# Kernel tuning notes

Hardware: AMD Instinct MI355X
Metric: run time of the kernel (lower is better)

Reference implementation:

```python
import jax, jax.numpy as jnp
import numpy as np

# --- FineRMoE routing constants (match init_kwargs) ---
TOP_K = 4
G_I, G_O = 2, 2
R_I, R_O = 4, 2
NUM_EXPERTS = 32  # must equal R_O*G_O*R_I*G_I


def _finermoe_router(scores):
    """scores: [T, E]. Returns (probs [T,top_k], selected [T,top_k])."""
    T, E = scores.shape
    S = E // (R_O * G_O)  # experts per concat-shard == R_I*G_I
    cs = scores.reshape(T, R_O * G_O, S)
    # top_k//G_O experts within each (R_O*G_O) shard
    _, add_idx = jax.lax.top_k(cs, TOP_K // G_O)
    add_mask = jnp.any(jax.nn.one_hot(add_idx, S, dtype=bool), axis=-2)  # [T, RO*GO, S]
    # keep the max-scoring R_O shard within each G_O group (argmax -> first max, like torch)
    shard_sum = cs.sum(-1).reshape(T, G_O, R_O)
    concat_mask = jax.nn.one_hot(jnp.argmax(shard_sum, axis=-1), R_O, dtype=bool)
    concat_mask = concat_mask.reshape(T, G_O * R_O)  # flat order matches RO*GO shard dim
    final_mask = (add_mask & concat_mask[:, :, None]).reshape(T, E)
    masked = jnp.where(final_mask, scores, -jnp.inf)
    probs, sel = jax.lax.top_k(masked, TOP_K)
    return probs, sel


def setup_inputs() -> dict:
    key = jax.random.key(0)
    ks = jax.random.split(key, 6)
    B, Sq, H, E, I = 1, 2048, 1024, NUM_EXPERTS, 256
    O = H // G_O  # expert output width
    return {
        "hidden_states": jax.random.normal(ks[0], (B, Sq, H), dtype=jnp.float32),
        "Wr": jax.random.normal(ks[1], (H, E), dtype=jnp.float32) * 0.02,
        "Wg": jax.random.normal(ks[2], (E, H, I), dtype=jnp.float32) * 0.02,
        "Wu": jax.random.normal(ks[3], (E, H, I), dtype=jnp.float32) * 0.02,
        "Wd": jax.random.normal(ks[4], (E, I, O), dtype=jnp.float32) * 0.02,
        "Wc": jax.random.normal(ks[5], (H, H), dtype=jnp.float32) * 0.02,
    }


def reference(hidden_states, Wr, Wg, Wu, Wd, Wc):
    B, Sq, H = hidden_states.shape
    T = B * Sq
    E = Wr.shape[1]
    x = hidden_states.reshape(T, H)
    router_logits = x @ Wr  # [T, E]
    probs, sel = _finermoe_router(router_logits)
    rw = jax.nn.softmax(probs.astype(jnp.float32), axis=1)
    rw = rw / rw.sum(-1, keepdims=True)  # norm_topk_prob
    rw = rw.astype(x.dtype)
    # dense combine weights [T, E] (zero for unselected experts)
    C = jnp.zeros((T, E), x.dtype).at[jnp.arange(T)[:, None], sel].add(rw)
    # all-expert MLP (stacked GEMMs); combine weights mask out unselected tokens
    h = jax.nn.silu(jnp.einsum('th,ehi->eti', x, Wg)) * jnp.einsum('th,ehi->eti', x, Wu)
    y = jnp.einsum('eti,eio->eto', h, Wd)  # [E, T, H//G_O]
    P = E // G_O  # experts per concat shard slice == R_O*G_I*R_I
    out = jnp.einsum('tgp,gpto->tgo', C.reshape(T, G_O, P),
                     y.reshape(G_O, P, T, H // G_O)).reshape(T, H)
    out = out @ Wc  # moe_concat_proj
    return out.reshape(B, Sq, H), router_logits
```

## Files before the change

### kernel.cpp

```cpp
#include <hip/hip_runtime.h>
#include <hip/hip_bf16.h>
#include <math.h>
#include <stdint.h>

typedef __hip_bfloat16 hbf16;

#define T_TOK 2048
#define H_DIM 1024
#define E_NUM 32
#define I_DIM 256
#define O_DIM 512
#define CAP   2048
#define TT    16
#define WT    16
#define XSTR2 520
#define HSTR  264
#define CSTR  32

typedef __bf16 bf16x8 __attribute__((ext_vector_type(8)));
typedef float  f32x4  __attribute__((ext_vector_type(4)));

__device__ __forceinline__ float b2f(hbf16 v) { return __bfloat162float(v); }
__device__ __forceinline__ float bb2f(ushort u) { return __uint_as_float((uint32_t)u << 16); }

__device__ __forceinline__ ushort f2b(float f) {
    uint32_t u = __float_as_uint(f);
    return (ushort)((u + 0x7FFFu + ((u >> 16) & 1u)) >> 16);
}

template<int BF>
__device__ __forceinline__ float ld(const void* p, size_t i) {
    if (BF) return b2f(((const hbf16*)p)[i]);
    else    return ((const float*)p)[i];
}

__device__ __forceinline__ f32x4 mfma_bf16(bf16x8 a, bf16x8 b, f32x4 c) {
    return __builtin_amdgcn_mfma_f32_16x16x32_bf16(a, b, c, 0, 0, 0);
}

__device__ __forceinline__ void sched_fence() { __builtin_amdgcn_sched_barrier(0); }

__global__ __launch_bounds__(256) void detect_kernel(
    const uint32_t* __restrict__ xw, int* __restrict__ flag, int* __restrict__ counts)
{
    __shared__ int cnt;
    if (threadIdx.x == 0) cnt = 0;
    if (threadIdx.x < E_NUM) counts[threadIdx.x * CSTR] = 0;
    __syncthreads();
    int c = 0;
    for (int i = threadIdx.x; i < 1024; i += 256) {
        int e = (xw[i] >> 7) & 0xFF;
        if (e >= 110 && e <= 140) c++;
    }
    atomicAdd(&cnt, c);
    __syncthreads();
    if (threadIdx.x == 0) *flag = (cnt > 512) ? 1 : 0;
}


__device__ void conv3_tile(const void* __restrict__ src, ushort* __restrict__ dst,
                           int bf, int K, int N, int b, float* __restrict__ sh)
{
    int tilesN = N >> 7, tilesK = K >> 5;
    int e  = b / (tilesK * tilesN);
    int r  = b % (tilesK * tilesN);
    int k0 = (r / tilesN) << 5;
    int n0 = (r % tilesN) << 7;
    size_t base = (size_t)e * K * N;
    int tid = threadIdx.x;
    {
        int row = tid >> 3, c0 = (tid & 7) * 16;
        if (!bf) {
            const float* sp = (const float*)src + base + (size_t)(k0 + row) * N + n0 + c0;
            #pragma unroll
            for (int i = 0; i < 4; ++i) {
                float4 v = *(const float4*)(sp + i * 4);
                sh[row * 132 + c0 + i*4 + 0] = v.x;
                sh[row * 132 + c0 + i*4 + 1] = v.y;
                sh[row * 132 + c0 + i*4 + 2] = v.z;
                sh[row * 132 + c0 + i*4 + 3] = v.w;
            }
        } else {
            const hbf16* sp = (const hbf16*)src + base + (size_t)(k0 + row) * N + n0 + c0;
            #pragma unroll
            for (int i = 0; i < 16; ++i) sh[row * 132 + c0 + i] = b2f(sp[i]);
        }
    }
    __syncthreads();
    {
        int nn = tid >> 1, kk = (tid & 1) * 16;
        union { ushort v[16]; uint4 u[2]; } R;
        #pragma unroll
        for (int i = 0; i < 16; ++i) R.v[i] = f2b(sh[(kk + i) * 132 + nn]);
        ushort* dp = dst + base + ((size_t)(k0 >> 5) * N + (n0 + nn)) * 32 + kk;
        *(uint4*)dp       = R.u[0];
        *(uint4*)(dp + 8) = R.u[1];
    }
    __syncthreads();
}

template<int BF>
__device__ void router3_body(const void* __restrict__ x, const void* __restrict__ Wr,
                             void* __restrict__ out_base,
                             int* __restrict__ counts, int* __restrict__ tok_list,
                             float* __restrict__ wt_list,
                             float* __restrict__ xs, float* __restrict__ sl,
                             float* __restrict__ sf, int t0)
{
    int tid  = threadIdx.x;
    int e    = tid & 31;
    int half = tid >> 5;

    {
        int t = tid >> 7;
        int c = (tid & 127) * 8;
        if (!BF) {
            const float* xp = (const float*)x + (size_t)(t0 + t) * H_DIM + c;
            *(float4*)&xs[t*1024 + c]     = *(const float4*)xp;
            *(float4*)&xs[t*1024 + c + 4] = *(const float4*)(xp + 4);
        } else {
            const hbf16* xp = (const hbf16*)x + (size_t)(t0 + t) * H_DIM + c;
            #pragma unroll
            for (int j = 0; j < 8; ++j) xs[t*1024 + c + j] = b2f(xp[j]);
        }
    }
    __syncthreads();

    float a0 = 0.f, a1 = 0.f;
    int kbase = half * 128;
    const float* xr0 = &xs[kbase];
    const float* xr1 = &xs[1024 + kbase];
    #pragma unroll 8
    for (int k = 0; k < 128; ++k) {
        float w = ld<BF>(Wr, (size_t)(kbase + k) * E_NUM + e);
        a0 = fmaf(xr0[k], w, a0);
        a1 = fmaf(xr1[k], w, a1);
    }
    sl[(0*8 + half)*32 + e] = a0;
    sl[(1*8 + half)*32 + e] = a1;
    __syncthreads();

    if (tid < 64) {
        int t  = tid >> 5;
        int ee = tid & 31;
        float s = 0.f;
        #pragma unroll
        for (int h = 0; h < 8; ++h) s += sl[(t*8 + h)*32 + ee];
        sf[t*32 + ee] = s;
        size_t li = (size_t)T_TOK * H_DIM + (size_t)(t0 + t) * E_NUM + ee;
        if (BF) ((hbf16*)out_base)[li] = __float2bfloat16(s);
        else    ((float*)out_base)[li] = s;
    }
    __syncthreads();

    if (tid < 2) {
        int t = t0 + tid;
        float s[E_NUM];
        #pragma unroll
        for (int i = 0; i < E_NUM; ++i) s[i] = sf[tid * 32 + i];

        int   selE[4];
        float selL[4];
        int ns = 0;
        for (int g = 0; g < 2; ++g) {
            float sum0 = 0.f, sum1 = 0.f;
            #pragma unroll
            for (int j = 0; j < 8; ++j) {
                sum0 += s[(2*g)   * 8 + j];
                sum1 += s[(2*g+1) * 8 + j];
            }
            int bestSh = (sum1 > sum0) ? (2*g+1) : (2*g);
            int base = bestSh * 8;
            int i1 = 0;
            for (int j = 1; j < 8; ++j) if (s[base+j] > s[base+i1]) i1 = j;
            int i2 = -1;
            for (int j = 0; j < 8; ++j) {
                if (j == i1) continue;
                if (i2 < 0 || s[base+j] > s[base+i2]) i2 = j;
            }
            selE[ns] = base + i1; selL[ns] = s[base+i1]; ++ns;
            selE[ns] = base + i2; selL[ns] = s[base+i2]; ++ns;
        }
        float m = fmaxf(fmaxf(selL[0], selL[1]), fmaxf(selL[2], selL[3]));
        float w[4];
        float sum = 0.f;
        for (int j = 0; j < 4; ++j) { w[j] = expf(selL[j] - m); sum += w[j]; }
        float inv = 1.f / sum;
        for (int j = 0; j < 4; ++j) {
            int ee = selE[j];
            int pos = atomicAdd(&counts[ee * CSTR], 1);
            if (pos >= 0 && pos < CAP) {
                tok_list[ee * CAP + pos] = t | (j << 11);
                wt_list[ee * CAP + pos]  = w[j] * inv;
            }
        }
    }
}

__global__ __launch_bounds__(256) void fused_cr_kernel(
    const void* x, const void* Wr,
    const void* Wg, const void* Wu, const void* Wd, const void* Wc,
    ushort* Wg_t, ushort* Wu_t, ushort* Wd_t, ushort* Wc_t,
    void* out_base, const int* __restrict__ flag,
    int* counts, int* tok_list, float* wt_list)
{
    __shared__ __align__(16) float sh[32 * 132];
    int b = blockIdx.x;
    if (b < 1024) {
        float* xs = sh;
        float* sl = sh + 2048;
        float* sf = sh + 2560;
        if (*flag) router3_body<1>(x, Wr, out_base, counts, tok_list, wt_list,
                                   xs, sl, sf, b * 2);
        else       router3_body<0>(x, Wr, out_base, counts, tok_list, wt_list,
                                   xs, sl, sf, b * 2);
    } else {
        int bb = b - 1024;
        int bf = *flag;
        if      (bb < 2048) conv3_tile(Wg, Wg_t, bf, 1024,  256, bb,        sh);
        else if (bb < 4096) conv3_tile(Wu, Wu_t, bf, 1024,  256, bb - 2048, sh);
        else if (bb < 5120) conv3_tile(Wd, Wd_t, bf,  256,  512, bb - 4096, sh);
        else                conv3_tile(Wc, Wc_t, bf, 1024, 1024, bb - 5120, sh);
    }
}

template<int BF>
__device__ void expert3_body(const void* __restrict__ x,
    const ushort* __restrict__ Wg_t, const ushort* __restrict__ Wu_t,
    const ushort* __restrict__ Wd_t,
    const int* __restrict__ counts, const int* __restrict__ tok_list,
    const float* __restrict__ wt_list, ushort* __restrict__ ybuf,
    ushort* __restrict__ xA, ushort* __restrict__ hsm,
    int* __restrict__ tokid, float* __restrict__ twt, int* __restrict__ tslot)
{
    int e = blockIdx.x;
    int n = counts[e * CSTR]; n = n < 0 ? 0 : (n > CAP ? CAP : n);
    int t0 = blockIdx.y * 32;
    if (t0 >= n) return;
    int tid  = threadIdx.x;
    int lane = tid & 63, wv = tid >> 6;
    int q = lane >> 4, l15 = lane & 15;

    if (tid < 32) {
        int it = t0 + tid;
        int id; float ww;
        if (it < n) { id = tok_list[e*CAP + it]; ww = wt_list[e*CAP + it]; }
        else        { id = tok_list[e*CAP + t0]; ww = 0.f; }
        tokid[tid] = id & 2047;
        tslot[tid] = (id >> 11) & 3;
        twt[tid]   = ww;
    }
    __syncthreads();

    const ushort* Bg0 = Wg_t + (size_t)e * (H_DIM * I_DIM) + (wv*32 + l15) * 32 + q*8;
    const ushort* Bu0 = Wu_t + (size_t)e * (H_DIM * I_DIM) + (wv*32 + l15) * 32 + q*8;

    f32x4 Cg[2][2], Cu[2][2];
    #pragma unroll
    for (int m = 0; m < 2; ++m)
        #pragma unroll
        for (int j = 0; j < 2; ++j) { Cg[m][j] = (f32x4)0.f; Cu[m][j] = (f32x4)0.f; }

    bf16x8 bg[2][4][2], bu[2][4][2];
    #pragma unroll
    for (int ig = 0; ig < 4; ++ig)
        #pragma unroll
        for (int j = 0; j < 2; ++j) {
            bg[0][ig][j] = *(const bf16x8*)(Bg0 + (size_t)ig*8192 + j*512);
            bu[0][ig][j] = *(const bf16x8*)(Bu0 + (size_t)ig*8192 + j*512);
        }
    sched_fence();

    #pragma unroll
    for (int hk = 0; hk < 2; ++hk) {
        if (hk) __syncthreads();

        {
            int row = tid >> 4;
            int kb  = (tid & 15) * 8;
            size_t srow = (size_t)tokid[row] * H_DIM + hk * 512;
            #pragma unroll
            for (int c = 0; c < 4; ++c) {
                int k = kb + c * 128;
                union { ushort v[8]; uint4 u; } U;
                if (BF) {
                    U.u = *(const uint4*)((const ushort*)x + srow + k);
                } else {
                    const float* xp = (const float*)x + srow + k;
                    float4 a = *(const float4*)xp;
                    float4 b = *(const float4*)(xp + 4);
                    U.v[0]=f2b(a.x); U.v[1]=f2b(a.y); U.v[2]=f2b(a.z); U.v[3]=f2b(a.w);
                    U.v[4]=f2b(b.x); U.v[5]=f2b(b.y); U.v[6]=f2b(b.z); U.v[7]=f2b(b.w);
                }
                *(uint4*)&xA[row * XSTR2 + k] = U.u;
            }
        }
        __syncthreads();

        #pragma unroll
        for (int g2 = 0; g2 < 4; ++g2) {
            int grp = hk * 4 + g2;
            int cb  = grp & 1;
            if (grp < 7) {
                #pragma unroll
                for (int ig = 0; ig < 4; ++ig)
                    #pragma unroll
                    for (int j = 0; j < 2; ++j) {
                        int idx = (grp + 1) * 4 + ig;
                        bg[cb^1][ig][j] = *(const bf16x8*)(Bg0 + (size_t)idx*8192 + j*512);
                        bu[cb^1][ig][j] = *(const bf16x8*)(Bu0 + (size_t)idx*8192 + j*512);
                    }
            }
            sched_fence();
            #pragma unroll
            for (int ig = 0; ig < 4; ++ig) {
                int kl = (g2 * 4 + ig) * 32;
                bf16x8 A0 = *(const bf16x8*)&xA[(l15)      * XSTR2 + kl + q*8];
                bf16x8 A1 = *(const bf16x8*)&xA[(16 + l15) * XSTR2 + kl + q*8];
                #pragma unroll
                for (int j = 0; j < 2; ++j) {
                    Cg[0][j] = mfma_bf16(A0, bg[cb][ig][j], Cg[0][j]);
                    Cg[1][j] = mfma_bf16(A1, bg[cb][ig][j], Cg[1][j]);
                    Cu[0][j] = mfma_bf16(A0, bu[cb][ig][j], Cu[0][j]);
                    Cu[1][j] = mfma_bf16(A1, bu[cb][ig][j], Cu[1][j]);
                }
            }
        }
    }

    const ushort* Bd0 = Wd_t + (size_t)e * (I_DIM * O_DIM) + (wv*64 + l15) * 32 + q*8;
    bf16x8 bd[2][4][4];
    #pragma unroll
    for (int g2 = 0; g2 < 2; ++g2)
        #pragma unroll
        for (int kc2 = 0; kc2 < 4; ++kc2)
            #pragma unroll
            for (int j = 0; j < 4; ++j)
                bd[g2][kc2][j] = *(const bf16x8*)(Bd0 + (size_t)(g2*4 + kc2)*16384 + j*512);
    sched_fence();

    #pragma unroll
    for (int m = 0; m < 2; ++m)
        #pragma unroll
        for (int j = 0; j < 2; ++j)
            #pragma unroll
            for (int r = 0; r < 4; ++r) {
                float g = Cg[m][j][r], u = Cu[m][j][r];
                float h = (g / (1.f + expf(-g))) * u;
                hsm[(m*16 + q*4 + r) * HSTR + wv*32 + j*16 + l15] = f2b(h);
            }
    __syncthreads();

    f32x4 Cd[2][4];
    #pragma unroll
    for (int m = 0; m < 2; ++m)
        #pragma unroll
        for (int j = 0; j < 4; ++j) Cd[m][j] = (f32x4)0.f;

    #pragma unroll
    for (int g2 = 0; g2 < 2; ++g2)
        #pragma unroll
        for (int kc2 = 0; kc2 < 4; ++kc2) {
            int kc = g2 * 4 + kc2;
            bf16x8 A0 = *(const bf16x8*)&hsm[(l15)      * HSTR + kc*32 + q*8];
            bf16x8 A1 = *(const bf16x8*)&hsm[(16 + l15) * HSTR + kc*32 + q*8];
            #pragma unroll
            for (int j = 0; j < 4; ++j) {
                Cd[0][j] = mfma_bf16(A0, bd[g2][kc2][j], Cd[0][j]);
                Cd[1][j] = mfma_bf16(A1, bd[g2][kc2][j], Cd[1][j]);
            }
        }

    #pragma unroll
    for (int m = 0; m < 2; ++m)
        #pragma unroll
        for (int r = 0; r < 4; ++r) {
            int row = m*16 + q*4 + r;
            if (t0 + row < n) {
                float ww = twt[row];
                size_t base = ((size_t)tokid[row] * 4 + tslot[row]) * O_DIM;
                #pragma unroll
                for (int j = 0; j < 4; ++j)
                    ybuf[base + wv*64 + j*16 + l15] = f2b(ww * Cd[m][j][r]);
            }
        }
}

__global__ __launch_bounds__(512, 2) void expert3_kernel(
    const void* x, const ushort* Wg_t, const ushort* Wu_t, const ushort* Wd_t,
    const int* flag, const int* counts, const int* tok_list, const float* wt_list,
    ushort* ybuf)
{
    __shared__ ushort xA[32 * XSTR2];
    __shared__ ushort hsm[32 * HSTR];
    __shared__ int    tokid[32];
    __shared__ float  twt[32];
    __shared__ int    tslot[32];
    if (*flag) expert3_body<1>(x, Wg_t, Wu_t, Wd_t, counts, tok_list, wt_list,
                               ybuf, xA, hsm, tokid, twt, tslot);
    else       expert3_body<0>(x, Wg_t, Wu_t, Wd_t, counts, tok_list, wt_list,
                               ybuf, xA, hsm, tokid, twt, tslot);
}

template<int BF>
__device__ void wc3_body(const ushort* __restrict__ ybuf, const ushort* __restrict__ Wc_t,
                         void* __restrict__ out_base, ushort* __restrict__ zA)
{
    int m0  = blockIdx.x * 32;
    int n0  = blockIdx.y * 256;
    int tid = threadIdx.x;
    int lane = tid & 63, wv = tid >> 6;
    int q = lane >> 4, l15 = lane & 15;

    const ushort* Bc0 = Wc_t + (size_t)(n0 + wv*32 + l15) * 32 + q*8;
    f32x4 C[2][2];
    #pragma unroll
    for (int m = 0; m < 2; ++m)
        #pragma unroll
        for (int j = 0; j < 2; ++j) C[m][j] = (f32x4)0.f;

    bf16x8 bc[2][4][2];
    #pragma unroll
    for (int ig = 0; ig < 4; ++ig)
        #pragma unroll
        for (int j = 0; j < 2; ++j)
            bc[0][ig][j] = *(const bf16x8*)(Bc0 + (size_t)ig*32768 + j*512);
    sched_fence();

    #pragma unroll
    for (int hk = 0; hk < 2; ++hk) {
        if (hk) __syncthreads();

        {
            int row = tid >> 4;
            int kb  = (tid & 15) * 8;
            int t = m0 + row;
            int s0 = hk ? 2 : 0;
            #pragma unroll
            for (int c = 0; c < 4; ++c) {
                int hl = kb + c * 128;
                const ushort* p0 = ybuf + ((size_t)t * 4 + s0) * O_DIM + hl;
                union { ushort v[8]; uint4 u; } A, B, R;
                A.u = *(const uint4*)p0;
                B.u = *(const uint4*)(p0 + O_DIM);
                #pragma unroll
                for (int i = 0; i < 8; ++i) R.v[i] = f2b(bb2f(A.v[i]) + bb2f(B.v[i]));
                *(uint4*)&zA[row * XSTR2 + hl] = R.u;
            }
        }
        __syncthreads();

        #pragma unroll
        for (int g2 = 0; g2 < 4; ++g2) {
            int grp = hk * 4 + g2;
            int cb  = grp & 1;
            if (grp < 7) {
                #pragma unroll
                for (int ig = 0; ig < 4; ++ig)
                    #pragma unroll
                    for (int j = 0; j < 2; ++j) {
                        int idx = (grp + 1) * 4 + ig;
                        bc[cb^1][ig][j] = *(const bf16x8*)(Bc0 + (size_t)idx*32768 + j*512);
                    }
            }
            sched_fence();
            #pragma unroll
            for (int ig = 0; ig < 4; ++ig) {
                int kl = (g2 * 4 + ig) * 32;
                bf16x8 A0 = *(const bf16x8*)&zA[(l15)      * XSTR2 + kl + q*8];
                bf16x8 A1 = *(const bf16x8*)&zA[(16 + l15) * XSTR2 + kl + q*8];
                #pragma unroll
                for (int j = 0; j < 2; ++j) {
                    C[0][j] = mfma_bf16(A0, bc[cb][ig][j], C[0][j]);
                    C[1][j] = mfma_bf16(A1, bc[cb][ig][j], C[1][j]);
                }
            }
        }
    }

    #pragma unroll
    for (int m = 0; m < 2; ++m)
        #pragma unroll
        for (int j = 0; j < 2; ++j)
            #pragma unroll
            for (int r = 0; r < 4; ++r) {
                int row = m0 + m*16 + q*4 + r;
                int col = n0 + wv*32 + j*16 + l15;
                size_t o = (size_t)row * H_DIM + col;
                if (BF) ((hbf16*)out_base)[o] = __float2bfloat16(C[m][j][r]);
                else    ((float*)out_base)[o] = C[m][j][r];
            }
}

__global__ __launch_bounds__(512, 2) void wc3_kernel(
    const ushort* ybuf, const ushort* Wc_t, void* out_base, const int* flag)
{
    __shared__ ushort zA[32 * XSTR2];
    if (*flag) wc3_body<1>(ybuf, Wc_t, out_base, zA);
    else       wc3_body<0>(ybuf, Wc_t, out_base, zA);
}


__global__ __launch_bounds__(256) void zero_kernel(
    float* __restrict__ z_fp32, float* __restrict__ z_bf16,
    const int* __restrict__ flag, int* __restrict__ counts)
{
    float* base = (*flag) ? z_bf16 : z_fp32;
    size_t i = (size_t)blockIdx.x * 256 + threadIdx.x;
    ((float4*)base)[i] = make_float4(0.f, 0.f, 0.f, 0.f);
    if (blockIdx.x == 0 && threadIdx.x < E_NUM) ((int*)counts)[threadIdx.x * CSTR] = 0;
}

template<int BF>
__device__ void router_body(const void* __restrict__ x, const void* __restrict__ Wr,
                            void* __restrict__ out_base,
                            int* __restrict__ counts, int* __restrict__ tok_list,
                            float* __restrict__ wt_list, float* __restrict__ sl)
{
    int t    = blockIdx.x;
    int lane = threadIdx.x;
    int e    = lane & 31;
    int half = lane >> 5;

    float acc = 0.f;
    size_t xoff = (size_t)t * H_DIM;
    int h0 = half * (H_DIM / 2);
    for (int h = h0; h < h0 + H_DIM / 2; ++h)
        acc = fmaf(ld<BF>(x, xoff + h), ld<BF>(Wr, (size_t)h * E_NUM + e), acc);
    acc += __shfl_down(acc, 32);

    if (lane < 32) {
        sl[e] = acc;
        size_t li = (size_t)T_TOK * H_DIM + (size_t)t * E_NUM + e;
        if (BF) ((hbf16*)out_base)[li] = __float2bfloat16(acc);
        else    ((float*)out_base)[li] = acc;
    }
    __syncthreads();

    if (lane == 0) {
        float s[E_NUM];
        #pragma unroll
        for (int i = 0; i < E_NUM; ++i) s[i] = sl[i];
        int   selE[4];
        float selL[4];
        int ns = 0;
        for (int g = 0; g < 2; ++g) {
            float sum0 = 0.f, sum1 = 0.f;
            #pragma unroll
            for (int j = 0; j < 8; ++j) {
                sum0 += s[(2*g)   * 8 + j];
                sum1 += s[(2*g+1) * 8 + j];
            }
            int bestSh = (sum1 > sum0) ? (2*g+1) : (2*g);
            int base = bestSh * 8;
            int i1 = 0;
            for (int j = 1; j < 8; ++j) if (s[base+j] > s[base+i1]) i1 = j;
            int i2 = -1;
            for (int j = 0; j < 8; ++j) {
                if (j == i1) continue;
                if (i2 < 0 || s[base+j] > s[base+i2]) i2 = j;
            }
            selE[ns] = base + i1; selL[ns] = s[base+i1]; ++ns;
            selE[ns] = base + i2; selL[ns] = s[base+i2]; ++ns;
        }
        float m = fmaxf(fmaxf(selL[0], selL[1]), fmaxf(selL[2], selL[3]));
        float w[4];
        float sum = 0.f;
        for (int j = 0; j < 4; ++j) { w[j] = expf(selL[j] - m); sum += w[j]; }
        float inv = 1.f / sum;
        for (int j = 0; j < 4; ++j) {
            int ee = selE[j];
            int pos = atomicAdd(&counts[ee * CSTR], 1);
            if (pos >= 0 && pos < CAP) {
                tok_list[ee * CAP + pos] = t;
                wt_list[ee * CAP + pos]  = w[j] * inv;
            }
        }
    }
}

__global__ __launch_bounds__(64) void router_kernel(
    const void* x, const void* Wr, void* out_base, const int* flag,
    int* counts, int* tok_list, float* wt_list)
{
    __shared__ float sl[E_NUM];
    if (*flag) router_body<1>(x, Wr, out_base, counts, tok_list, wt_list, sl);
    else       router_body<0>(x, Wr, out_base, counts, tok_list, wt_list, sl);
}

template<int BF>
__device__ void expert_body(const void* __restrict__ x,
                            const void* __restrict__ Wg, const void* __restrict__ Wu,
                            const void* __restrict__ Wd,
                            const int* __restrict__ counts, const int* __restrict__ tok_list,
                            const float* __restrict__ wt_list,
                            float* __restrict__ z, float* __restrict__ xsbuf)
{
    int e = blockIdx.x;
    int n = counts[e * CSTR];
    n = n < 0 ? 0 : (n > CAP ? CAP : n);
    int t0 = blockIdx.y * TT;
    if (t0 >= n) return;
    int tid = threadIdx.x;

    float (*xs)[H_DIM] = reinterpret_cast<float(*)[H_DIM]>(xsbuf);
    float (*hs)[I_DIM] = reinterpret_cast<float(*)[I_DIM]>(xsbuf);

    const int*   tl = tok_list + e * CAP;
    const float* wl = wt_list  + e * CAP;

    for (int idx = tid; idx < TT * H_DIM; idx += 256) {
        int tt = idx >> 10;
        int h  = idx & (H_DIM - 1);
        int it = t0 + tt;
        int tkn = (it < n) ? tl[it] : tl[t0];
        tkn = (tkn < 0) ? 0 : (tkn >= T_TOK ? T_TOK - 1 : tkn);
        xs[tt][h] = ld<BF>(x, (size_t)tkn * H_DIM + h);
    }
    __syncthreads();

    size_t wbase = (size_t)e * H_DIM * I_DIM + tid;
    float ag[TT], au[TT];
    #pragma unroll
    for (int tt = 0; tt < TT; ++tt) { ag[tt] = 0.f; au[tt] = 0.f; }

    for (int k = 0; k < H_DIM; k += 4) {
        float g0 = ld<BF>(Wg, wbase + (size_t)(k+0) * I_DIM);
        float g1 = ld<BF>(Wg, wbase + (size_t)(k+1) * I_DIM);
        float g2 = ld<BF>(Wg, wbase + (size_t)(k+2) * I_DIM);
        float g3 = ld<BF>(Wg, wbase + (size_t)(k+3) * I_DIM);
        float u0 = ld<BF>(Wu, wbase + (size_t)(k+0) * I_DIM);
        float u1 = ld<BF>(Wu, wbase + (size_t)(k+1) * I_DIM);
        float u2 = ld<BF>(Wu, wbase + (size_t)(k+2) * I_DIM);
        float u3 = ld<BF>(Wu, wbase + (size_t)(k+3) * I_DIM);
        #pragma unroll
        for (int tt = 0; tt < TT; ++tt) {
            float4 xv = *(const float4*)&xs[tt][k];
            ag[tt] = fmaf(xv.w, g3, fmaf(xv.z, g2, fmaf(xv.y, g1, fmaf(xv.x, g0, ag[tt]))));
            au[tt] = fmaf(xv.w, u3, fmaf(xv.z, u2, fmaf(xv.y, u1, fmaf(xv.x, u0, au[tt]))));
        }
    }
    float hval[TT];
    #pragma unroll
    for (int tt = 0; tt < TT; ++tt) {
        float g = ag[tt];
        hval[tt] = (g / (1.f + expf(-g))) * au[tt];
    }
    __syncthreads();
    #pragma unroll
    for (int tt = 0; tt < TT; ++tt) hs[tt][tid] = hval[tt];
    __syncthreads();

    size_t dbase = (size_t)e * I_DIM * O_DIM;
    float y0[TT], y1[TT];
    #pragma unroll
    for (int tt = 0; tt < TT; ++tt) { y0[tt] = 0.f; y1[tt] = 0.f; }

    for (int k = 0; k < I_DIM; k += 4) {
        float d00 = ld<BF>(Wd, dbase + (size_t)(k+0) * O_DIM + tid);
        float d01 = ld<BF>(Wd, dbase + (size_t)(k+1) * O_DIM + tid);
        float d02 = ld<BF>(Wd, dbase + (size_t)(k+2) * O_DIM + tid);
        float d03 = ld<BF>(Wd, dbase + (size_t)(k+3) * O_DIM + tid);
        float d10 = ld<BF>(Wd, dbase + (size_t)(k+0) * O_DIM + tid + 256);
        float d11 = ld<BF>(Wd, dbase + (size_t)(k+1) * O_DIM + tid + 256);
        float d12 = ld<BF>(Wd, dbase + (size_t)(k+2) * O_DIM + tid + 256);
        float d13 = ld<BF>(Wd, dbase + (size_t)(k+3) * O_DIM + tid + 256);
        #pragma unroll
        for (int tt = 0; tt < TT; ++tt) {
            float4 hv = *(const float4*)&hs[tt][k];
            y0[tt] = fmaf(hv.w, d03, fmaf(hv.z, d02, fmaf(hv.y, d01, fmaf(hv.x, d00, y0[tt]))));
            y1[tt] = fmaf(hv.w, d13, fmaf(hv.z, d12, fmaf(hv.y, d11, fmaf(hv.x, d10, y1[tt]))));
        }
    }

    int gsel = e >> 4;
    size_t colbase = (size_t)gsel * O_DIM;
    #pragma unroll
    for (int tt = 0; tt < TT; ++tt) {
        int it = t0 + tt;
        if (it < n) {
            float w  = wl[it];
            int tkn = tl[it];
            tkn = (tkn < 0) ? 0 : (tkn >= T_TOK ? T_TOK - 1 : tkn);
            atomicAdd(&z[(size_t)tkn * H_DIM + colbase + tid],       w * y0[tt]);
            atomicAdd(&z[(size_t)tkn * H_DIM + colbase + tid + 256], w * y1[tt]);
        }
    }
}

__global__ __launch_bounds__(256) void expert_kernel(
    const void* x, const void* Wg, const void* Wu, const void* Wd,
    const int* flag, const int* counts, const int* tok_list, const float* wt_list,
    float* z_fp32, float* z_bf16)
{
    __shared__ __align__(16) float xsbuf[TT * H_DIM];
    if (*flag) expert_body<1>(x, Wg, Wu, Wd, counts, tok_list, wt_list, z_bf16, xsbuf);
    else       expert_body<0>(x, Wg, Wu, Wd, counts, tok_list, wt_list, z_fp32, xsbuf);
}

template<int BF>
__device__ void wc_body(const float* __restrict__ z, const void* __restrict__ Wc,
                        void* __restrict__ out_base, float* __restrict__ psbuf)
{
    int t0  = blockIdx.x * WT;
    int tid = threadIdx.x;
    float (*ps)[H_DIM] = reinterpret_cast<float(*)[H_DIM]>(psbuf);

    for (int idx = tid; idx < WT * H_DIM; idx += 256) {
        int tt = idx >> 10;
        int h  = idx & (H_DIM - 1);
        ps[tt][h] = z[(size_t)(t0 + tt) * H_DIM + h];
    }
    __syncthreads();

    float acc[WT][4];
    #pragma unroll
    for (int tt = 0; tt < WT; ++tt)
        #pragma unroll
        for (int qq = 0; qq < 4; ++qq) acc[tt][qq] = 0.f;

    for (int k = 0; k < H_DIM; k += 2) {
        float c00 = ld<BF>(Wc, (size_t)(k+0) * H_DIM + tid);
        float c01 = ld<BF>(Wc, (size_t)(k+0) * H_DIM + tid + 256);
        float c02 = ld<BF>(Wc, (size_t)(k+0) * H_DIM + tid + 512);
        float c03 = ld<BF>(Wc, (size_t)(k+0) * H_DIM + tid + 768);
        float c10 = ld<BF>(Wc, (size_t)(k+1) * H_DIM + tid);
        float c11 = ld<BF>(Wc, (size_t)(k+1) * H_DIM + tid + 256);
        float c12 = ld<BF>(Wc, (size_t)(k+1) * H_DIM + tid + 512);
        float c13 = ld<BF>(Wc, (size_t)(k+1) * H_DIM + tid + 768);
        #pragma unroll
        for (int tt = 0; tt < WT; ++tt) {
            float2 pv = *(const float2*)&ps[tt][k];
            acc[tt][0] = fmaf(pv.y, c10, fmaf(pv.x, c00, acc[tt][0]));
            acc[tt][1] = fmaf(pv.y, c11, fmaf(pv.x, c01, acc[tt][1]));
            acc[tt][2] = fmaf(pv.y, c12, fmaf(pv.x, c02, acc[tt][2]));
            acc[tt][3] = fmaf(pv.y, c13, fmaf(pv.x, c03, acc[tt][3]));
        }
    }

    #pragma unroll
    for (int tt = 0; tt < WT; ++tt) {
        #pragma unroll
        for (int qq = 0; qq < 4; ++qq) {
            size_t o = (size_t)(t0 + tt) * H_DIM + tid + 256 * qq;
            if (BF) ((hbf16*)out_base)[o] = __float2bfloat16(acc[tt][qq]);
            else    ((float*)out_base)[o] = acc[tt][qq];
        }
    }
}

__global__ __launch_bounds__(256) void wc_kernel(
    const float* z_fp32, const float* z_bf16, const void* Wc,
    void* out_base, const int* flag)
{
    __shared__ __align__(16) float psbuf[WT * H_DIM];
    if (*flag) wc_body<1>(z_bf16, Wc, out_base, psbuf);
    else       wc_body<0>(z_fp32, Wc, out_base, psbuf);
}

extern "C" void kernel_launch(void* const* d_in, const int* in_sizes, int n_in,
                              void* d_out, int out_size, void* d_ws, size_t ws_size,
                              hipStream_t stream)
{
    (void)in_sizes; (void)n_in; (void)out_size;

    const void* x  = d_in[0];
    const void* Wr = d_in[1];
    const void* Wg = d_in[2];
    const void* Wu = d_in[3];
    const void* Wd = d_in[4];
    const void* Wc = d_in[5];

    char* ws = (char*)d_ws;
    int*   counts   = (int*)(ws + 0);
    int*   flag     = (int*)(ws + 4096);
    int*   tok_list = (int*)(ws + 8192);
    float* wt_list  = (float*)(ws + 8192 + (size_t)E_NUM * CAP * 4);

    detect_kernel<<<1, 256, 0, stream>>>((const uint32_t*)x, flag, counts);

    if (ws_size >= ((size_t)58 << 20)) {
        ushort* ybuf = (ushort*)(ws + ((size_t)1  << 20));
        ushort* Wg_t = (ushort*)(ws + ((size_t)16 << 20));
        ushort* Wu_t = (ushort*)(ws + ((size_t)32 << 20));
        ushort* Wd_t = (ushort*)(ws + ((size_t)48 << 20));
        ushort* Wc_t = (ushort*)(ws + ((size_t)56 << 20));

        fused_cr_kernel<<<1024 + 5376, 256, 0, stream>>>(
            x, Wr, Wg, Wu, Wd, Wc, Wg_t, Wu_t, Wd_t, Wc_t,
            d_out, flag, counts, tok_list, wt_list);
        expert3_kernel<<<dim3(E_NUM, T_TOK / 32), 512, 0, stream>>>(
            x, Wg_t, Wu_t, Wd_t, flag, counts, tok_list, wt_list, ybuf);
        wc3_kernel<<<dim3(T_TOK / 32, 4), 512, 0, stream>>>(ybuf, Wc_t, d_out, flag);
    } else {
        float* z_bf16 = (float*)(ws + (1u << 20));
        float* z_fp32 = (float*)d_out;
        zero_kernel<<<T_TOK, 256, 0, stream>>>(z_fp32, z_bf16, flag, counts);
        router_kernel<<<T_TOK, 64, 0, stream>>>(x, Wr, d_out, flag, counts, tok_list, wt_list);
        expert_kernel<<<dim3(E_NUM, T_TOK / TT), 256, 0, stream>>>(
            x, Wg, Wu, Wd, flag, counts, tok_list, wt_list, z_fp32, z_bf16);
        wc_kernel<<<T_TOK / WT, 256, 0, stream>>>(z_fp32, z_bf16, Wc, d_out, flag);
    }
}
```

Measured before the change: 210.0 us.

## Deepen weight prefetch to triple buffering and widen Wc GEMM blocks to 1024 threads

```diff
diff --git a/kernel.cpp b/kernel.cpp
--- a/kernel.cpp
+++ b/kernel.cpp
@@ -261,14 +261,17 @@
         #pragma unroll
         for (int j = 0; j < 2; ++j) { Cg[m][j] = (f32x4)0.f; Cu[m][j] = (f32x4)0.f; }
 
-    bf16x8 bg[2][4][2], bu[2][4][2];
-    #pragma unroll
-    for (int ig = 0; ig < 4; ++ig)
-        #pragma unroll
-        for (int j = 0; j < 2; ++j) {
-            bg[0][ig][j] = *(const bf16x8*)(Bg0 + (size_t)ig*8192 + j*512);
-            bu[0][ig][j] = *(const bf16x8*)(Bu0 + (size_t)ig*8192 + j*512);
-        }
+    bf16x8 bg[3][4][2], bu[3][4][2];
+    #pragma unroll
+    for (int p = 0; p < 2; ++p)
+        #pragma unroll
+        for (int ig = 0; ig < 4; ++ig)
+            #pragma unroll
+            for (int j = 0; j < 2; ++j) {
+                int idx = p * 4 + ig;
+                bg[p][ig][j] = *(const bf16x8*)(Bg0 + (size_t)idx*8192 + j*512);
+                bu[p][ig][j] = *(const bf16x8*)(Bu0 + (size_t)idx*8192 + j*512);
+            }
     sched_fence();
 
     #pragma unroll
@@ -300,18 +303,20 @@
         #pragma unroll
         for (int g2 = 0; g2 < 4; ++g2) {
             int grp = hk * 4 + g2;
-            int cb  = grp & 1;
-            if (grp < 7) {
+            int pf  = grp + 2;
+            if (pf < 8) {
+                int pb = pf % 3;
                 #pragma unroll
                 for (int ig = 0; ig < 4; ++ig)
                     #pragma unroll
                     for (int j = 0; j < 2; ++j) {
-                        int idx = (grp + 1) * 4 + ig;
-                        bg[cb^1][ig][j] = *(const bf16x8*)(Bg0 + (size_t)idx*8192 + j*512);
-                        bu[cb^1][ig][j] = *(const bf16x8*)(Bu0 + (size_t)idx*8192 + j*512);
+                        int idx = pf * 4 + ig;
+                        bg[pb][ig][j] = *(const bf16x8*)(Bg0 + (size_t)idx*8192 + j*512);
+                        bu[pb][ig][j] = *(const bf16x8*)(Bu0 + (size_t)idx*8192 + j*512);
                     }
             }
             sched_fence();
+            int cb = grp % 3;
             #pragma unroll
             for (int ig = 0; ig < 4; ++ig) {
                 int kl = (g2 * 4 + ig) * 32;
@@ -412,19 +417,16 @@
     int lane = tid & 63, wv = tid >> 6;
     int q = lane >> 4, l15 = lane & 15;
 
-    const ushort* Bc0 = Wc_t + (size_t)(n0 + wv*32 + l15) * 32 + q*8;
-    f32x4 C[2][2];
-    #pragma unroll
-    for (int m = 0; m < 2; ++m)
-        #pragma unroll
-        for (int j = 0; j < 2; ++j) C[m][j] = (f32x4)0.f;
-
-    bf16x8 bc[2][4][2];
-    #pragma unroll
-    for (int ig = 0; ig < 4; ++ig)
-        #pragma unroll
-        for (int j = 0; j < 2; ++j)
-            bc[0][ig][j] = *(const bf16x8*)(Bc0 + (size_t)ig*32768 + j*512);
+    const ushort* Bc0 = Wc_t + (size_t)(n0 + wv*16 + l15) * 32 + q*8;
+    f32x4 C[2];
+    C[0] = (f32x4)0.f; C[1] = (f32x4)0.f;
+
+    bf16x8 bc[3][4];
+    #pragma unroll
+    for (int p = 0; p < 2; ++p)
+        #pragma unroll
+        for (int ig = 0; ig < 4; ++ig)
+            bc[p][ig] = *(const bf16x8*)(Bc0 + (size_t)(p*4 + ig)*32768);
     sched_fence();
 
     #pragma unroll
@@ -432,13 +434,13 @@
         if (hk) __syncthreads();
 
         {
-            int row = tid >> 4;
-            int kb  = (tid & 15) * 8;
+            int row = tid >> 5;
+            int kb  = (tid & 31) * 8;
             int t = m0 + row;
             int s0 = hk ? 2 : 0;
             #pragma unroll
-            for (int c = 0; c < 4; ++c) {
-                int hl = kb + c * 128;
+            for (int c = 0; c < 2; ++c) {
+                int hl = kb + c * 256;
                 const ushort* p0 = ybuf + ((size_t)t * 4 + s0) * O_DIM + hl;
                 union { ushort v[8]; uint4 u; } A, B, R;
                 A.u = *(const uint4*)p0;
@@ -453,27 +455,22 @@
         #pragma unroll
         for (int g2 = 0; g2 < 4; ++g2) {
             int grp = hk * 4 + g2;
-            int cb  = grp & 1;
-            if (grp < 7) {
+            int pf  = grp + 2;
+            if (pf < 8) {
+                int pb = pf % 3;
                 #pragma unroll
                 for (int ig = 0; ig < 4; ++ig)
-                    #pragma unroll
-                    for (int j = 0; j < 2; ++j) {
-                        int idx = (grp + 1) * 4 + ig;
-                        bc[cb^1][ig][j] = *(const bf16x8*)(Bc0 + (size_t)idx*32768 + j*512);
-                    }
+                    bc[pb][ig] = *(const bf16x8*)(Bc0 + (size_t)(pf*4 + ig)*32768);
             }
             sched_fence();
+            int cb = grp % 3;
             #pragma unroll
             for (int ig = 0; ig < 4; ++ig) {
                 int kl = (g2 * 4 + ig) * 32;
                 bf16x8 A0 = *(const bf16x8*)&zA[(l15)      * XSTR2 + kl + q*8];
                 bf16x8 A1 = *(const bf16x8*)&zA[(16 + l15) * XSTR2 + kl + q*8];
-                #pragma unroll
-                for (int j = 0; j < 2; ++j) {
-                    C[0][j] = mfma_bf16(A0, bc[cb][ig][j], C[0][j]);
-                    C[1][j] = mfma_bf16(A1, bc[cb][ig][j], C[1][j]);
-                }
+                C[0] = mfma_bf16(A0, bc[cb][ig], C[0]);
+                C[1] = mfma_bf16(A1, bc[cb][ig], C[1]);
             }
         }
     }
@@ -481,18 +478,16 @@
     #pragma unroll
     for (int m = 0; m < 2; ++m)
         #pragma unroll
-        for (int j = 0; j < 2; ++j)
-            #pragma unroll
-            for (int r = 0; r < 4; ++r) {
-                int row = m0 + m*16 + q*4 + r;
-                int col = n0 + wv*32 + j*16 + l15;
-                size_t o = (size_t)row * H_DIM + col;
-                if (BF) ((hbf16*)out_base)[o] = __float2bfloat16(C[m][j][r]);
-                else    ((float*)out_base)[o] = C[m][j][r];
-            }
-}
-
-__global__ __launch_bounds__(512, 2) void wc3_kernel(
+        for (int r = 0; r < 4; ++r) {
+            int row = m0 + m*16 + q*4 + r;
+            int col = n0 + wv*16 + l15;
+            size_t o = (size_t)row * H_DIM + col;
+            if (BF) ((hbf16*)out_base)[o] = __float2bfloat16(C[m][r]);
+            else    ((float*)out_base)[o] = C[m][r];
+        }
+}
+
+__global__ __launch_bounds__(1024, 4) void wc3_kernel(
     const ushort* ybuf, const ushort* Wc_t, void* out_base, const int* flag)
 {
     __shared__ ushort zA[32 * XSTR2];
@@ -791,7 +786,7 @@
             d_out, flag, counts, tok_list, wt_list);
         expert3_kernel<<<dim3(E_NUM, T_TOK / 32), 512, 0, stream>>>(
             x, Wg_t, Wu_t, Wd_t, flag, counts, tok_list, wt_list, ybuf);
-        wc3_kernel<<<dim3(T_TOK / 32, 4), 512, 0, stream>>>(ybuf, Wc_t, d_out, flag);
+        wc3_kernel<<<dim3(T_TOK / 32, 4), 1024, 0, stream>>>(ybuf, Wc_t, d_out, flag);
     } else {
         float* z_bf16 = (float*)(ws + (1u << 20));
         float* z_fp32 = (float*)d_out;
```

After: 210.3 us. Within noise of the previous version (+0.2%).
